# Performance work log

Hardware: AMD Instinct MI355X
Metric: run time of the kernel (lower is better)

Reference implementation:

```python
import jax, jax.numpy as jnp
import numpy as np

T, N, E = 6, 50000, 1600000
NFEAT, NHID, NCLASS = 256, 256, 16
SLOPE = 11.0 / 48.0  # eval-mode RReLU: mean of default (lower=1/8, upper=1/3)


def _grcu(H_seq, src, dst, val, Wz, Uz, bz, Wr, Ur, br, Wh, Uh, bh, Q0):
    """One GRCU layer: matrix-GRU weight evolution + sparse GCN aggregation per step.
    H_seq: [T, N, in]  src/dst: [T, E] int  val: [T, E]  Q0: [in, out]."""
    n = H_seq.shape[1]

    def step(Q, xs):
        H, s, d, v = xs
        # mat_GRU_cell: x = hidden = prev_Q (z_topk path is unused in this repo's forward)
        z = jax.nn.sigmoid(Wz @ Q + Uz @ Q + bz)
        r = jax.nn.sigmoid(Wr @ Q + Ur @ Q + br)
        h = jnp.tanh(Wh @ Q + Uh @ (r * Q) + bh)
        Qn = (1.0 - z) * Q + z * h
        XW = H @ Qn                                   # [N, out]
        msg = v[:, None] * XW[s]                      # per-edge gather: Ahat row weights
        agg = jax.ops.segment_sum(msg, d, num_segments=n)  # Ahat @ (H @ Qn)
        out = jnp.where(agg >= 0, agg, SLOPE * agg)   # RReLU (eval)
        return Qn, out

    _, out_seq = jax.lax.scan(step, Q0, (H_seq, src, dst, val))
    return out_seq  # [T, N, out]


def setup_inputs() -> dict:
    key = jax.random.key(0)
    ks = iter(jax.random.split(key, 64))

    def rn(shape, scale=0.05):
        return jax.random.normal(next(ks), shape, dtype=jnp.float32) * scale

    inp = {
        "node_feats": jax.random.normal(next(ks), (T, N, NFEAT), dtype=jnp.float32),
        "edge_val": jax.random.uniform(next(ks), (T, E), dtype=jnp.float32),
    }
    for l, (fi, fo) in enumerate([(NFEAT, NHID), (NHID, NHID)]):
        for g in ("z", "r", "h"):
            inp[f"l{l}_W{g}"] = rn((fi, fi))
            inp[f"l{l}_U{g}"] = rn((fi, fi))
            inp[f"l{l}_b{g}"] = jnp.zeros((fi, fo), dtype=jnp.float32)
        inp[f"l{l}_Q0"] = rn((fi, fo))
    inp["mlp_W1"] = rn((NHID, NHID))
    inp["mlp_b1"] = jnp.zeros((NHID,), dtype=jnp.float32)
    inp["mlp_W2"] = rn((NHID, NCLASS))
    inp["mlp_b2"] = jnp.zeros((NCLASS,), dtype=jnp.float32)
    inp["edge_src"] = jax.random.randint(next(ks), (T, E), 0, N, dtype=jnp.int32)
    inp["edge_dst"] = jax.random.randint(next(ks), (T, E), 0, N, dtype=jnp.int32)
    return inp


def reference(node_feats, edge_val,
              l0_Wz, l0_Uz, l0_bz, l0_Wr, l0_Ur, l0_br, l0_Wh, l0_Uh, l0_bh, l0_Q0,
              l1_Wz, l1_Uz, l1_bz, l1_Wr, l1_Ur, l1_br, l1_Wh, l1_Uh, l1_bh, l1_Q0,
              mlp_W1, mlp_b1, mlp_W2, mlp_b2,
              edge_src, edge_dst):
    h1 = _grcu(node_feats, edge_src, edge_dst, edge_val,
               l0_Wz, l0_Uz, l0_bz, l0_Wr, l0_Ur, l0_br, l0_Wh, l0_Uh, l0_bh, l0_Q0)
    h2 = _grcu(h1, edge_src, edge_dst, edge_val,
               l1_Wz, l1_Uz, l1_bz, l1_Wr, l1_Ur, l1_br, l1_Wh, l1_Uh, l1_bh, l1_Q0)
    out = h2[-1]                                    # last timestep, [N, nhid]
    hid = jax.nn.relu(out @ mlp_W1 + mlp_b1)
    logits = hid @ mlp_W2 + mlp_b2
    return jax.nn.log_softmax(logits, axis=1)       # [N, nclass]
```

## Files before the change

### kernel.cpp

```cpp
#include <hip/hip_runtime.h>
#include <cstddef>

#define SLOPE_F (11.0f / 48.0f)

static const int NN = 50000;
static const int EE = 1600000;
static const int D  = 256;
static const int NCH = 196;
static const int GB  = 391;

typedef __attribute__((ext_vector_type(8))) short short8;
typedef __attribute__((ext_vector_type(4))) float f32x4;
typedef __attribute__((ext_vector_type(2))) float f32x2;

__device__ __forceinline__ ushort f2bf(float f) {
    unsigned u = __float_as_uint(f);
    unsigned r = (u + 0x7fffu + ((u >> 16) & 1u)) >> 16;
    return (ushort)r;
}
__device__ __forceinline__ float bf2f(ushort u) {
    return __uint_as_float(((unsigned)u) << 16);
}

__device__ __forceinline__ unsigned enc8(float x) {
    unsigned ux = __float_as_uint(x);
    unsigned sign = (ux >> 31) << 7;
    float ax = __uint_as_float(ux & 0x7fffffffu);
    if (!(ax < 448.f)) return sign | 0x7E;
    if (ax < 0.015625f) {
        int m = (int)(ax * 512.f + 0.5f);
        if (m > 7) return sign | 0x08;
        return sign | m;
    }
    unsigned u = __float_as_uint(ax);
    u += 0x7FFFFu + ((u >> 20) & 1u);
    int e = (int)((u >> 23) & 255) - 127 + 7;
    if (e > 15) return sign | 0x7E;
    return sign | (e << 3) | ((u >> 20) & 7);
}

__global__ __launch_bounds__(256) void prephist_kernel(
        const float* __restrict__ Wz0, const float* __restrict__ Uz0,
        const float* __restrict__ Wr0, const float* __restrict__ Ur0,
        const float* __restrict__ Wh0, const float* __restrict__ Uh0,
        const float* __restrict__ Wz1, const float* __restrict__ Uz1,
        const float* __restrict__ Wr1, const float* __restrict__ Ur1,
        const float* __restrict__ Wh1, const float* __restrict__ Uh1,
        const float* __restrict__ W1,
        ushort* __restrict__ WB, ushort* __restrict__ BtW1,
        const int* __restrict__ dst, int* __restrict__ D8,
        ushort* __restrict__ rank) {
    int b = blockIdx.x;
    int tid = threadIdx.x;
    if (b >= 144) {
        int e = (b - 144) * 256 + tid;
        if (e < EE) {
            int d = dst[e];
            rank[e] = (ushort)atomicAdd(&D8[(e & 7) * NN + d], 1);
        }
        return;
    }
    __shared__ float lt[64][65];
    if (b < 128) {
        int mat = b >> 4;
        int tr = (b >> 2) & 3, tc = b & 3;
        const float* P = nullptr; const float* S = nullptr;
        switch (mat) {
            case 0: P = Wz0; S = Uz0; break;
            case 1: P = Wr0; S = Ur0; break;
            case 2: P = Wh0; break;
            case 3: P = Uh0; break;
            case 4: P = Wz1; S = Uz1; break;
            case 5: P = Wr1; S = Ur1; break;
            case 6: P = Wh1; break;
            default: P = Uh1; break;
        }
#pragma unroll
        for (int r0 = 0; r0 < 64; r0 += 4) {
            int r = r0 + (tid >> 6);
            int c = tid & 63;
            int row = tr * 64 + r, col = tc * 64 + c;
            float v = P[row * 256 + col];
            if (S) v += S[row * 256 + col];
            lt[r][c] = v;
        }
        __syncthreads();
#pragma unroll
        for (int c0 = 0; c0 < 64; c0 += 4) {
            int c = c0 + (tid >> 6);
            int r = tid & 63;
            WB[(size_t)mat * 65536 + (size_t)(tc * 64 + c) * 256 + tr * 64 + r] =
                f2bf(lt[r][c]);
        }
    } else {
        int t = b - 128;
        int tr = (t >> 2) & 3, tc = t & 3;
#pragma unroll
        for (int r0 = 0; r0 < 64; r0 += 4) {
            int r = r0 + (tid >> 6);
            int c = tid & 63;
            lt[r][c] = W1[(tr * 64 + r) * 256 + tc * 64 + c];
        }
        __syncthreads();
#pragma unroll
        for (int c0 = 0; c0 < 64; c0 += 4) {
            int c = c0 + (tid >> 6);
            int r = tid & 63;
            BtW1[(size_t)(tc * 64 + c) * 256 + tr * 64 + r] = f2bf(lt[r][c]);
        }
    }
}

__global__ __launch_bounds__(256) void gruscan_kernel(
        const ushort* __restrict__ WB,
        const float* __restrict__ bz0, const float* __restrict__ br0,
        const float* __restrict__ bh0, const float* __restrict__ Q00,
        const float* __restrict__ bz1, const float* __restrict__ br1,
        const float* __restrict__ bh1, const float* __restrict__ Q01,
        ushort* __restrict__ Bt,
        const int* __restrict__ D8, int* __restrict__ rs, int* __restrict__ base8,
        int* __restrict__ bsum, int* __restrict__ boff, int* __restrict__ done) {
    int tid = threadIdx.x;
    if (blockIdx.x >= 512) {
        __shared__ int wsum[4];
        __shared__ int lastflag;
        int blk = blockIdx.x - 512;
        int i = blk * 256 + tid;
        int lane = tid & 63, wv = tid >> 6;
        int c[8];
        int v = 0;
#pragma unroll
        for (int r = 0; r < 8; ++r) {
            c[r] = (i < NN) ? D8[r * NN + i] : 0;
            v += c[r];
        }
        int x = v;
#pragma unroll
        for (int off = 1; off < 64; off <<= 1) {
            int t = __shfl_up(x, off, 64);
            if (lane >= off) x += t;
        }
        if (lane == 63) wsum[wv] = x;
        __syncthreads();
        if (tid == 0) {
            int s = 0;
#pragma unroll
            for (int q = 0; q < 4; ++q) { int t = wsum[q]; wsum[q] = s; s += t; }
            bsum[blk] = s;
        }
        __syncthreads();
        if (i < NN) {
            int p = wsum[wv] + x - v;
            rs[i] = p;
            int b = p;
            int4 b0, b1;
            b0.x = b; b += c[0]; b0.y = b; b += c[1];
            b0.z = b; b += c[2]; b0.w = b; b += c[3];
            b1.x = b; b += c[4]; b1.y = b; b += c[5];
            b1.z = b; b += c[6]; b1.w = b;
            *(int4*)&base8[8 * i]     = b0;
            *(int4*)&base8[8 * i + 4] = b1;
        }
        __threadfence();
        if (tid == 0) lastflag = (atomicAdd(done, 1) == NCH - 1);
        __syncthreads();
        if (lastflag) {
            __threadfence();
            int bv = (tid < NCH) ? bsum[tid] : 0;
            int bx = bv;
#pragma unroll
            for (int off = 1; off < 64; off <<= 1) {
                int t = __shfl_up(bx, off, 64);
                if (lane >= off) bx += t;
            }
            if (lane == 63) wsum[wv] = bx;
            __syncthreads();
            if (tid == 0) {
                int s = 0;
#pragma unroll
                for (int q = 0; q < 4; ++q) { int t = wsum[q]; wsum[q] = s; s += t; }
            }
            __syncthreads();
            if (tid < NCH) boff[tid] = wsum[wv] + bx - bv;
        }
        return;
    }
    __shared__ float qs[256];
    __shared__ float rqs[256];
    int layer = blockIdx.x >> 8;
    int j = blockIdx.x & 255;
    int i = tid;
    const ushort* Mz = WB + ((size_t)layer * 4 + 0) * 65536;
    const ushort* Mr = WB + ((size_t)layer * 4 + 1) * 65536;
    const ushort* Wh = WB + ((size_t)layer * 4 + 2) * 65536;
    const ushort* Uh = WB + ((size_t)layer * 4 + 3) * 65536;
    const float* bz = layer ? bz1 : bz0;
    const float* br = layer ? br1 : br0;
    const float* bh = layer ? bh1 : bh0;
    const float* Q0 = layer ? Q01 : Q00;

    float bzv = bz[i * 256 + j];
    float brv = br[i * 256 + j];
    float bhv = bh[i * 256 + j];

    qs[i] = Q0[i * 256 + j];
    __syncthreads();

    for (int step = 0; step < 6; ++step) {
        float az = 0.f, ar = 0.f, ah = 0.f;
#pragma unroll 8
        for (int k = 0; k < 256; ++k) {
            float q = qs[k];
            az += bf2f(Mz[k * 256 + i]) * q;
            ar += bf2f(Mr[k * 256 + i]) * q;
            ah += bf2f(Wh[k * 256 + i]) * q;
        }
        float zz = 1.f / (1.f + expf(-(az + bzv)));
        float rr = 1.f / (1.f + expf(-(ar + brv)));
        float qo = qs[i];
        rqs[i] = rr * qo;
        __syncthreads();
        float bu = 0.f;
#pragma unroll 8
        for (int k = 0; k < 256; ++k)
            bu += bf2f(Uh[k * 256 + i]) * rqs[k];
        float h = tanhf(ah + bu + bhv);
        float qn = (1.f - zz) * qo + zz * h;
        __syncthreads();
        qs[i] = qn;
        __syncthreads();
    }
    Bt[(size_t)layer * 65536 + (size_t)j * 256 + i] = f2bf(qs[i]);
}

template <int ASRC>
__device__ __forceinline__ void gemm_body(int bid, int tid,
                                          const ushort* __restrict__ A,
                                          const float* __restrict__ Af,
                                          const ushort* __restrict__ Bt,
                                          unsigned char* __restrict__ C8, int M) {
    int w = tid >> 6, l = tid & 63;
    int lr = l & 15;
    int lk = l >> 4;
    int row0 = bid * 128 + w * 32;
    int ra = row0 + lr;      if (ra > M - 1) ra = M - 1;
    int rb = row0 + 16 + lr; if (rb > M - 1) rb = M - 1;
    const ushort* Ap0  = A  + (size_t)ra * 256 + lk * 8;
    const ushort* Ap1  = A  + (size_t)rb * 256 + lk * 8;
    const float*  Apf0 = Af + (size_t)ra * 256 + lk * 8;
    const float*  Apf1 = Af + (size_t)rb * 256 + lk * 8;
    const ushort* Bp   = Bt + (size_t)lr * 256 + lk * 8;

    f32x4 acc0[16] = {};
    f32x4 acc1[16] = {};
#pragma unroll
    for (int kc = 0; kc < 8; ++kc) {
        short8 a0, a1;
        if (ASRC == 0) {
            a0 = *(const short8*)(Ap0 + kc * 32);
            a1 = *(const short8*)(Ap1 + kc * 32);
        } else {
            float4 f0 = *(const float4*)(Apf0 + kc * 32);
            float4 f1 = *(const float4*)(Apf0 + kc * 32 + 4);
            float4 g0 = *(const float4*)(Apf1 + kc * 32);
            float4 g1 = *(const float4*)(Apf1 + kc * 32 + 4);
            a0[0] = (short)f2bf(f0.x); a0[1] = (short)f2bf(f0.y);
            a0[2] = (short)f2bf(f0.z); a0[3] = (short)f2bf(f0.w);
            a0[4] = (short)f2bf(f1.x); a0[5] = (short)f2bf(f1.y);
            a0[6] = (short)f2bf(f1.z); a0[7] = (short)f2bf(f1.w);
            a1[0] = (short)f2bf(g0.x); a1[1] = (short)f2bf(g0.y);
            a1[2] = (short)f2bf(g0.z); a1[3] = (short)f2bf(g0.w);
            a1[4] = (short)f2bf(g1.x); a1[5] = (short)f2bf(g1.y);
            a1[6] = (short)f2bf(g1.z); a1[7] = (short)f2bf(g1.w);
        }
#pragma unroll
        for (int nb = 0; nb < 16; ++nb) {
            short8 bf = *(const short8*)(Bp + (size_t)nb * 4096 + kc * 32);
            acc0[nb] = __builtin_amdgcn_mfma_f32_16x16x32_bf16(a0, bf, acc0[nb], 0, 0, 0);
            acc1[nb] = __builtin_amdgcn_mfma_f32_16x16x32_bf16(a1, bf, acc1[nb], 0, 0, 0);
        }
    }

    int ro = lk * 4;
#pragma unroll
    for (int q = 0; q < 4; ++q) {
        unsigned w0[4], w1[4];
#pragma unroll
        for (int t = 0; t < 4; ++t) {
            unsigned x0 = 0, x1 = 0;
#pragma unroll
            for (int u = 0; u < 4; ++u) {
                x0 |= enc8(acc0[t * 4 + u][q]) << (8 * u);
                x1 |= enc8(acc1[t * 4 + u][q]) << (8 * u);
            }
            w0[t] = x0; w1[t] = x1;
        }
        int g0 = row0 + ro + q;
        if (g0 < M)
            *(uint4*)&C8[(size_t)g0 * 256 + lr * 16] = make_uint4(w0[0], w0[1], w0[2], w0[3]);
        int g1 = row0 + 16 + ro + q;
        if (g1 < M)
            *(uint4*)&C8[(size_t)g1 * 256 + lr * 16] = make_uint4(w1[0], w1[1], w1[2], w1[3]);
    }
}

__global__ __launch_bounds__(256) void gemm_mfma(const ushort* __restrict__ A,
                                                 const ushort* __restrict__ Bt,
                                                 unsigned char* __restrict__ C8, int M) {
    gemm_body<0>(blockIdx.x, threadIdx.x, A, nullptr, Bt, C8, M);
}

__global__ __launch_bounds__(256) void gemsca_kernel(const float* __restrict__ Af,
                                                     const ushort* __restrict__ Bt,
                                                     unsigned char* __restrict__ C8, int M,
                                                     const int* __restrict__ src,
                                                     const int* __restrict__ dst,
                                                     const float* __restrict__ val,
                                                     const int* __restrict__ base8,
                                                     const int* __restrict__ boff,
                                                     const ushort* __restrict__ rank,
                                                     unsigned* __restrict__ csr) {
    if (blockIdx.x < GB) {
        gemm_body<1>(blockIdx.x, threadIdx.x, nullptr, Af, Bt, C8, M);
        return;
    }
    int e = (blockIdx.x - GB) * 256 + threadIdx.x;
    if (e < EE) {
        int d = dst[e];
        int p = base8[8 * d + (e & 7)] + boff[d >> 8] + (int)rank[e];
        unsigned pk = (unsigned)src[e] | ((unsigned)f2bf(val[e]) << 16);
        __builtin_nontemporal_store(pk, &csr[p]);
    }
}

__global__ __launch_bounds__(256) void gemm2_kernel(const ushort* __restrict__ A,
                                                    const ushort* __restrict__ Bt,
                                                    const float* __restrict__ bias,
                                                    const float* __restrict__ W2,
                                                    const float* __restrict__ b2,
                                                    float* __restrict__ out, int M) {
    __shared__ ushort Hl[128 * 264];
    int tid = threadIdx.x;
    int w = tid >> 6, l = tid & 63;
    int lr = l & 15;
    int lk = l >> 4;
    int row0 = blockIdx.x * 128 + w * 32;
    int ra = row0 + lr;      if (ra > M - 1) ra = M - 1;
    int rb = row0 + 16 + lr; if (rb > M - 1) rb = M - 1;
    const ushort* Ap0 = A + (size_t)ra * 256 + lk * 8;
    const ushort* Ap1 = A + (size_t)rb * 256 + lk * 8;
    const ushort* Bp  = Bt + (size_t)lr * 256 + lk * 8;

    f32x4 acc0[16] = {};
    f32x4 acc1[16] = {};
#pragma unroll
    for (int kc = 0; kc < 8; ++kc) {
        short8 a0 = *(const short8*)(Ap0 + kc * 32);
        short8 a1 = *(const short8*)(Ap1 + kc * 32);
#pragma unroll
        for (int nb = 0; nb < 16; ++nb) {
            short8 bf = *(const short8*)(Bp + (size_t)nb * 4096 + kc * 32);
            acc0[nb] = __builtin_amdgcn_mfma_f32_16x16x32_bf16(a0, bf, acc0[nb], 0, 0, 0);
            acc1[nb] = __builtin_amdgcn_mfma_f32_16x16x32_bf16(a1, bf, acc1[nb], 0, 0, 0);
        }
    }

    int ro = lk * 4;
    int lrow0 = w * 32;
#pragma unroll
    for (int nb = 0; nb < 16; ++nb) {
        int gc = nb * 16 + lr;
        float bb = bias[gc];
#pragma unroll
        for (int q = 0; q < 4; ++q) {
            Hl[(lrow0 + ro + q) * 264 + gc]      = f2bf(fmaxf(acc0[nb][q] + bb, 0.f));
            Hl[(lrow0 + 16 + ro + q) * 264 + gc] = f2bf(fmaxf(acc1[nb][q] + bb, 0.f));
        }
    }
    __syncthreads();

    int c = tid & 15;
    float b2v = b2[c];
#pragma unroll
    for (int it = 0; it < 8; ++it) {
        int r = it * 16 + (tid >> 4);
        int g = blockIdx.x * 128 + r;
        const ushort* hp = &Hl[r * 264];
        float acc2 = b2v;
        for (int k8 = 0; k8 < 32; ++k8) {
            short8 h8 = *(const short8*)(hp + k8 * 8);
#pragma unroll
            for (int u = 0; u < 8; ++u)
                acc2 += bf2f((ushort)h8[u]) * W2[(k8 * 8 + u) * 16 + c];
        }
        float m = acc2;
#pragma unroll
        for (int off = 1; off < 16; off <<= 1)
            m = fmaxf(m, __shfl_xor(m, off, 16));
        float ex = expf(acc2 - m);
        float s = ex;
#pragma unroll
        for (int off = 1; off < 16; off <<= 1)
            s += __shfl_xor(s, off, 16);
        if (g < M) out[(size_t)g * 16 + c] = acc2 - m - logf(s);
    }
}

__global__ __launch_bounds__(256) void agg_csr_kernel(const unsigned char* __restrict__ XW,
                                                      const unsigned* __restrict__ csr,
                                                      const int* __restrict__ rs,
                                                      const int* __restrict__ boff,
                                                      ushort* __restrict__ out) {
    int d = blockIdx.x * 4 + (threadIdx.x >> 6);
    if (d >= NN) return;
    int l = threadIdx.x & 63;
    int h = l >> 5;
    int il = l & 31;
    int beg = rs[d] + boff[d >> 8];
    int end = (d + 1 < NN) ? (rs[d + 1] + boff[(d + 1) >> 8]) : EE;
    float a0 = 0.f, a1 = 0.f, a2 = 0.f, a3 = 0.f;
    float a4 = 0.f, a5 = 0.f, a6 = 0.f, a7 = 0.f;
    int i = beg + h;
    for (; i + 14 < end; i += 16) {
        unsigned e[8];
        uint2 x[8];
#pragma unroll
        for (int u = 0; u < 8; ++u) e[u] = csr[i + 2 * u];
#pragma unroll
        for (int u = 0; u < 8; ++u)
            x[u] = *(const uint2*)&XW[(size_t)(e[u] & 0xffffu) * 256 + il * 8];
#pragma unroll
        for (int u = 0; u < 8; ++u) {
            float v = bf2f((ushort)(e[u] >> 16));
            f32x2 p0 = __builtin_amdgcn_cvt_pk_f32_fp8(x[u].x, false);
            f32x2 p1 = __builtin_amdgcn_cvt_pk_f32_fp8(x[u].x, true);
            f32x2 p2 = __builtin_amdgcn_cvt_pk_f32_fp8(x[u].y, false);
            f32x2 p3 = __builtin_amdgcn_cvt_pk_f32_fp8(x[u].y, true);
            a0 += v * p0.x; a1 += v * p0.y; a2 += v * p1.x; a3 += v * p1.y;
            a4 += v * p2.x; a5 += v * p2.y; a6 += v * p3.x; a7 += v * p3.y;
        }
    }
    for (; i < end; i += 2) {
        unsigned e0 = csr[i];
        float v = bf2f((ushort)(e0 >> 16));
        uint2 x0 = *(const uint2*)&XW[(size_t)(e0 & 0xffffu) * 256 + il * 8];
        f32x2 p0 = __builtin_amdgcn_cvt_pk_f32_fp8(x0.x, false);
        f32x2 p1 = __builtin_amdgcn_cvt_pk_f32_fp8(x0.x, true);
        f32x2 p2 = __builtin_amdgcn_cvt_pk_f32_fp8(x0.y, false);
        f32x2 p3 = __builtin_amdgcn_cvt_pk_f32_fp8(x0.y, true);
        a0 += v * p0.x; a1 += v * p0.y; a2 += v * p1.x; a3 += v * p1.y;
        a4 += v * p2.x; a5 += v * p2.y; a6 += v * p3.x; a7 += v * p3.y;
    }
    a0 += __shfl_xor(a0, 32); a1 += __shfl_xor(a1, 32);
    a2 += __shfl_xor(a2, 32); a3 += __shfl_xor(a3, 32);
    a4 += __shfl_xor(a4, 32); a5 += __shfl_xor(a5, 32);
    a6 += __shfl_xor(a6, 32); a7 += __shfl_xor(a7, 32);
    if (h == 0) {
        float r[8] = {a0, a1, a2, a3, a4, a5, a6, a7};
#pragma unroll
        for (int u = 0; u < 8; ++u) {
            int p = il * 8 + u;
            int c = ((p & 15) << 4) | (p >> 4);
            float v = r[u];
            v = (v >= 0.f) ? v : SLOPE_F * v;
            out[(size_t)d * D + c] = f2bf(v);
        }
    }
}

extern "C" void kernel_launch(void* const* d_in, const int* in_sizes, int n_in,
                              void* d_out, int out_size, void* d_ws, size_t ws_size,
                              hipStream_t stream) {
    const float* node_feats = (const float*)d_in[0];
    const float* edge_val   = (const float*)d_in[1];
    const float* l0_Wz = (const float*)d_in[2];
    const float* l0_Uz = (const float*)d_in[3];
    const float* l0_bz = (const float*)d_in[4];
    const float* l0_Wr = (const float*)d_in[5];
    const float* l0_Ur = (const float*)d_in[6];
    const float* l0_br = (const float*)d_in[7];
    const float* l0_Wh = (const float*)d_in[8];
    const float* l0_Uh = (const float*)d_in[9];
    const float* l0_bh = (const float*)d_in[10];
    const float* l0_Q0 = (const float*)d_in[11];
    const float* l1_Wz = (const float*)d_in[12];
    const float* l1_Uz = (const float*)d_in[13];
    const float* l1_bz = (const float*)d_in[14];
    const float* l1_Wr = (const float*)d_in[15];
    const float* l1_Ur = (const float*)d_in[16];
    const float* l1_br = (const float*)d_in[17];
    const float* l1_Wh = (const float*)d_in[18];
    const float* l1_Uh = (const float*)d_in[19];
    const float* l1_bh = (const float*)d_in[20];
    const float* l1_Q0 = (const float*)d_in[21];
    const float* W1 = (const float*)d_in[22];
    const float* b1 = (const float*)d_in[23];
    const float* W2 = (const float*)d_in[24];
    const float* b2 = (const float*)d_in[25];
    const int* e_src = (const int*)d_in[26];
    const int* e_dst = (const int*)d_in[27];
    float* out = (float*)d_out;

    const size_t BIG = (size_t)NN * D;
    unsigned char* XW8 = (unsigned char*)d_ws;
    ushort* H   = (ushort*)(XW8 + BIG);
    ushort* Bt  = H + BIG;
    ushort* WB  = Bt + 3 * 65536;
    unsigned* csr = (unsigned*)(WB + 8 * 65536);
    int*    D8  = (int*)(csr + EE);
    int*    done = D8 + 8 * NN;
    int*    rs  = done + 4;
    int*    base8 = rs + NN;
    int*    bsum = base8 + 8 * NN;
    int*    boff = bsum + 200;
    ushort* rank = (ushort*)(boff + 200);

    const float* feats5 = node_feats + (size_t)5 * BIG;
    const int*   src5   = e_src + (size_t)5 * EE;
    const int*   dst5   = e_dst + (size_t)5 * EE;
    const float* val5   = edge_val + (size_t)5 * EE;

    hipMemsetAsync(D8, 0, (8 * NN + 1) * sizeof(int), stream);

    const int histblocks = (EE + 255) / 256;
    prephist_kernel<<<144 + histblocks, 256, 0, stream>>>(
        l0_Wz, l0_Uz, l0_Wr, l0_Ur, l0_Wh, l0_Uh,
        l1_Wz, l1_Uz, l1_Wr, l1_Ur, l1_Wh, l1_Uh,
        W1, WB, Bt + 2 * 65536, dst5, D8, rank);

    gruscan_kernel<<<512 + NCH, 256, 0, stream>>>(WB, l0_bz, l0_br, l0_bh, l0_Q0,
                                                  l1_bz, l1_br, l1_bh, l1_Q0, Bt,
                                                  D8, rs, base8, bsum, boff, done);

    gemsca_kernel<<<GB + histblocks, 256, 0, stream>>>(feats5, Bt + 0 * 65536, XW8, NN,
                                                       src5, dst5, val5, base8, boff,
                                                       rank, csr);

    const int ablocks = (NN + 3) / 4;

    agg_csr_kernel<<<ablocks, 256, 0, stream>>>(XW8, csr, rs, boff, H);

    gemm_mfma<<<GB, 256, 0, stream>>>(H, Bt + 1 * 65536, XW8, NN);

    agg_csr_kernel<<<ablocks, 256, 0, stream>>>(XW8, csr, rs, boff, H);

    gemm2_kernel<<<GB, 256, 0, stream>>>(H, Bt + 2 * 65536, b1, W2, b2, out, NN);
}
```

Baseline: 571.7 us.

## Split CSR aggregation into four feature slices launched as separate blocks

The aggregation kernel now splits the 256-byte fp8 feature row into four 64-byte column slices, each handled by its own set of blocks, so the grid grows fourfold. Within a wavefront, 16 lanes cover one slice and four edge groups run in parallel, with a two-step shuffle reduction at the end. The aim is a per-slice gathered working set that fits better in L2/MALL and more parallelism per node. The cost is that every CSR index and row offset is read four times, each gather is only 4 bytes per lane, and the kernel launches more blocks.

```diff
diff --git a/kernel.cpp b/kernel.cpp
--- a/kernel.cpp
+++ b/kernel.cpp
@@ -8,6 +8,7 @@
 static const int D  = 256;
 static const int NCH = 196;
 static const int GB  = 391;
+static const int ABLK = 12500;
 
 typedef __attribute__((ext_vector_type(8))) short short8;
 typedef __attribute__((ext_vector_type(4))) float f32x4;
@@ -411,55 +412,52 @@
                                                       const int* __restrict__ rs,
                                                       const int* __restrict__ boff,
                                                       ushort* __restrict__ out) {
-    int d = blockIdx.x * 4 + (threadIdx.x >> 6);
+    int bid = blockIdx.x;
+    int slice = bid / ABLK;
+    int dblk = bid - slice * ABLK;
+    int d = dblk * 4 + (threadIdx.x >> 6);
     if (d >= NN) return;
     int l = threadIdx.x & 63;
-    int h = l >> 5;
-    int il = l & 31;
+    int h = l >> 4;
+    int il = l & 15;
+    const unsigned char* XWs = XW + slice * 64 + il * 4;
     int beg = rs[d] + boff[d >> 8];
     int end = (d + 1 < NN) ? (rs[d + 1] + boff[(d + 1) >> 8]) : EE;
     float a0 = 0.f, a1 = 0.f, a2 = 0.f, a3 = 0.f;
-    float a4 = 0.f, a5 = 0.f, a6 = 0.f, a7 = 0.f;
     int i = beg + h;
-    for (; i + 14 < end; i += 16) {
-        unsigned e[8];
-        uint2 x[8];
-#pragma unroll
-        for (int u = 0; u < 8; ++u) e[u] = csr[i + 2 * u];
-#pragma unroll
-        for (int u = 0; u < 8; ++u)
-            x[u] = *(const uint2*)&XW[(size_t)(e[u] & 0xffffu) * 256 + il * 8];
-#pragma unroll
-        for (int u = 0; u < 8; ++u) {
+    for (; i + 12 < end; i += 16) {
+        unsigned e[4];
+        unsigned x[4];
+#pragma unroll
+        for (int u = 0; u < 4; ++u) e[u] = csr[i + 4 * u];
+#pragma unroll
+        for (int u = 0; u < 4; ++u)
+            x[u] = *(const unsigned*)(XWs + (size_t)(e[u] & 0xffffu) * 256);
+#pragma unroll
+        for (int u = 0; u < 4; ++u) {
             float v = bf2f((ushort)(e[u] >> 16));
-            f32x2 p0 = __builtin_amdgcn_cvt_pk_f32_fp8(x[u].x, false);
-            f32x2 p1 = __builtin_amdgcn_cvt_pk_f32_fp8(x[u].x, true);
-            f32x2 p2 = __builtin_amdgcn_cvt_pk_f32_fp8(x[u].y, false);
-            f32x2 p3 = __builtin_amdgcn_cvt_pk_f32_fp8(x[u].y, true);
+            f32x2 p0 = __builtin_amdgcn_cvt_pk_f32_fp8(x[u], false);
+            f32x2 p1 = __builtin_amdgcn_cvt_pk_f32_fp8(x[u], true);
             a0 += v * p0.x; a1 += v * p0.y; a2 += v * p1.x; a3 += v * p1.y;
-            a4 += v * p2.x; a5 += v * p2.y; a6 += v * p3.x; a7 += v * p3.y;
-        }
-    }
-    for (; i < end; i += 2) {
+        }
+    }
+    for (; i < end; i += 4) {
         unsigned e0 = csr[i];
         float v = bf2f((ushort)(e0 >> 16));
-        uint2 x0 = *(const uint2*)&XW[(size_t)(e0 & 0xffffu) * 256 + il * 8];
-        f32x2 p0 = __builtin_amdgcn_cvt_pk_f32_fp8(x0.x, false);
-        f32x2 p1 = __builtin_amdgcn_cvt_pk_f32_fp8(x0.x, true);
-        f32x2 p2 = __builtin_amdgcn_cvt_pk_f32_fp8(x0.y, false);
-        f32x2 p3 = __builtin_amdgcn_cvt_pk_f32_fp8(x0.y, true);
+        unsigned x0 = *(const unsigned*)(XWs + (size_t)(e0 & 0xffffu) * 256);
+        f32x2 p0 = __builtin_amdgcn_cvt_pk_f32_fp8(x0, false);
+        f32x2 p1 = __builtin_amdgcn_cvt_pk_f32_fp8(x0, true);
         a0 += v * p0.x; a1 += v * p0.y; a2 += v * p1.x; a3 += v * p1.y;
-        a4 += v * p2.x; a5 += v * p2.y; a6 += v * p3.x; a7 += v * p3.y;
-    }
-    a0 += __shfl_xor(a0, 32); a1 += __shfl_xor(a1, 32);
-    a2 += __shfl_xor(a2, 32); a3 += __shfl_xor(a3, 32);
-    a4 += __shfl_xor(a4, 32); a5 += __shfl_xor(a5, 32);
-    a6 += __shfl_xor(a6, 32); a7 += __shfl_xor(a7, 32);
+    }
+    a0 += __shfl_xor(a0, 16); a0 += __shfl_xor(a0, 32);
+    a1 += __shfl_xor(a1, 16); a1 += __shfl_xor(a1, 32);
+    a2 += __shfl_xor(a2, 16); a2 += __shfl_xor(a2, 32);
+    a3 += __shfl_xor(a3, 16); a3 += __shfl_xor(a3, 32);
     if (h == 0) {
-        float r[8] = {a0, a1, a2, a3, a4, a5, a6, a7};
-#pragma unroll
-        for (int u = 0; u < 8; ++u) {
-            int p = il * 8 + u;
+        float r[4] = {a0, a1, a2, a3};
+#pragma unroll
+        for (int u = 0; u < 4; ++u) {
+            int p = slice * 64 + il * 4 + u;
             int c = ((p & 15) << 4) | (p >> 4);
             float v = r[u];
             v = (v >= 0.f) ? v : SLOPE_F * v;
@@ -536,13 +534,11 @@
                                                        src5, dst5, val5, base8, boff,
                                                        rank, csr);
 
-    const int ablocks = (NN + 3) / 4;
-
-    agg_csr_kernel<<<ablocks, 256, 0, stream>>>(XW8, csr, rs, boff, H);
+    agg_csr_kernel<<<4 * ABLK, 256, 0, stream>>>(XW8, csr, rs, boff, H);
 
     gemm_mfma<<<GB, 256, 0, stream>>>(H, Bt + 1 * 65536, XW8, NN);
 
-    agg_csr_kernel<<<ablocks, 256, 0, stream>>>(XW8, csr, rs, boff, H);
+    agg_csr_kernel<<<4 * ABLK, 256, 0, stream>>>(XW8, csr, rs, boff, H);
 
     gemm2_kernel<<<GB, 256, 0, stream>>>(H, Bt + 2 * 65536, b1, W2, b2, out, NN);
 }
```

Measured after the change: 674.5 us. +18.0%, slower.
